# Kernel optimization log

Hardware: AMD Instinct MI355X
Metric: run time of the kernel (lower is better)

## Reference

```python
import jax, jax.numpy as jnp
import numpy as np

N, D, N_CLASSES = 8192, 512, 128
POS_MARGIN = 1.0  # default path: sample_method=None, Dynamic_margin=None


def setup_inputs() -> dict:
    key = jax.random.key(0)
    k1, k2 = jax.random.split(key)
    x = jax.random.normal(k1, (N, D), dtype=jnp.float32)
    # metric-learning embeddings are L2-normalized so sim in [-1, 1]
    x = x / jnp.linalg.norm(x, axis=1, keepdims=True)
    targets = jax.random.randint(k2, (N,), 0, N_CLASSES, dtype=jnp.int64)
    return {"inputs": x, "targets": targets, "nonorm": 0}


def reference(inputs, targets, nonorm):
    n = inputs.shape[0]
    sim = jnp.matmul(inputs, inputs.T)                      # [n, n]
    same = targets[:, None] == targets[None, :]             # [n, n]
    pos_mask = same & (sim < POS_MARGIN)                    # drops self-sim == 1
    neg_mask = ~same

    # per-row masked log-sum-exp (sort in original is irrelevant to the sums)
    pos_sum = jnp.sum(jnp.where(pos_mask, jnp.exp(1.0 - sim), 0.0), axis=1)
    neg_sum = jnp.sum(jnp.where(neg_mask, jnp.exp(sim), 0.0), axis=1)
    pos_loss = jnp.log(pos_sum)
    neg_loss = jnp.log(neg_sum)

    has_neg = jnp.any(neg_mask, axis=1)                     # rows w/o negs are skipped
    loss = jnp.sum(jnp.where(has_neg, pos_loss + neg_loss, 0.0)) / n
    prec = jnp.mean(1.0 - has_neg.astype(jnp.float32))      # fraction of skipped rows

    # torch code reports means of the LAST row's pos/neg pairs
    last_pos = pos_mask[-1]
    last_neg = neg_mask[-1]
    mean_pos_sim = jnp.sum(jnp.where(last_pos, sim[-1], 0.0)) / jnp.sum(last_pos)
    mean_neg_sim = jnp.sum(jnp.where(last_neg, sim[-1], 0.0)) / jnp.sum(last_neg)
    return loss, prec, mean_pos_sim, mean_neg_sim
```

## Files before the change

### kernel.cpp

```cpp
#include <hip/hip_runtime.h>
#include <math.h>

#define N_ 8192
#define D_ 512
#define NC_ 128
#define T32 32
#define BK_ 64
#define KSTEPS 8

typedef __attribute__((ext_vector_type(8))) short bf16x8;
typedef __attribute__((ext_vector_type(4))) float f32x4;
typedef __attribute__((ext_vector_type(4))) unsigned short us4;

static __device__ __forceinline__ unsigned short f2bf(float f) {
    union { float f; unsigned u; } c; c.f = f;
    unsigned u = c.u;
    u += 0x7fffu + ((u >> 16) & 1u);
    return (unsigned short)(u >> 16);
}

__global__ __launch_bounds__(256) void k_pre(const float* __restrict__ x,
                                             unsigned short* __restrict__ xb,
                                             const int* __restrict__ tg,
                                             double* __restrict__ sim_last,
                                             int* __restrict__ hist32,
                                             double* __restrict__ gd,
                                             int* __restrict__ gi) {
    const int bid = blockIdx.x;
    const int tid = threadIdx.x;
    if (bid == 0 && tid == 0) {
        atomicExch((unsigned long long*)&gd[0], 0ull);
        atomicExch((unsigned long long*)&gd[1], 0ull);
        atomicExch((unsigned long long*)&gd[2], 0ull);
        atomicExch(&gi[0], 0); atomicExch(&gi[1], 0);
        atomicExch(&gi[2], 0); atomicExch(&gi[3], 0);
    }
    if (bid < 4096) {
        int i = bid * 256 + tid;
        float4 v = reinterpret_cast<const float4*>(x)[i];
        us4 o = { f2bf(v.x), f2bf(v.y), f2bf(v.z), f2bf(v.w) };
        reinterpret_cast<us4*>(xb)[i] = o;
    } else if (bid < 6144) {
        int j    = (bid - 4096) * 4 + (tid >> 6);
        int lane = tid & 63;
        const float* xl = x + (size_t)(N_ - 1) * D_;
        const float* xj = x + (size_t)j * D_;
        double acc = 0.0;
#pragma unroll
        for (int it = 0; it < 8; ++it) {
            int k = it * 64 + lane;
            acc += (double)xl[k] * (double)xj[k];
        }
#pragma unroll
        for (int m = 32; m >= 1; m >>= 1) acc += __shfl_xor(acc, m, 64);
        if (lane == 0) sim_last[j] = acc;
    } else {
        __shared__ int lh[NC_];
        int b = bid - 6144;
        if (tid < NC_) lh[tid] = 0;
        __syncthreads();
        atomicAdd(&lh[tg[b * 256 + tid]], 1);
        __syncthreads();
        if (tid < NC_) hist32[b * NC_ + tid] = lh[tid];
    }
}

__global__ __launch_bounds__(512, 1) void k_main(const unsigned short* __restrict__ xb,
                                                 const int* __restrict__ tg,
                                                 float* __restrict__ bufP,
                                                 float* __restrict__ bufN) {
    __shared__ alignas(16) unsigned short As0_[2 * 256 * 64];
    __shared__ alignas(16) unsigned short Bs0_[2 * 256 * 64];

    const int tid  = threadIdx.x;
    const int w    = tid >> 6;
    const int lane = tid & 63;
    const int q    = lane >> 4;
    const int l15  = lane & 15;
    const int wrow = w >> 2;
    const int wcol = w & 3;

    const int bswz = (blockIdx.x & 7) * 66 + (blockIdx.x >> 3);

    int rem = bswz;
    int it = 0;
    while (rem >= (T32 - it)) { rem -= (T32 - it); it++; }
    const int jt = it + rem;
    const int row0 = it * 256;
    const int col0 = jt * 256;

    auto stage_tile = [&](int p, int kt) {
        const int k0 = kt * BK_;
#pragma unroll
        for (int set = 0; set < 4; ++set) {
            int ls = set * 4096 + tid * 8;
            int r  = ls >> 6;
            int sl = (ls >> 3) & 7;
            int g  = sl ^ (r & 7);
            const unsigned short* ga = xb + (size_t)(row0 + r) * D_ + k0 + g * 8;
            const unsigned short* gb = xb + (size_t)(col0 + r) * D_ + k0 + g * 8;
            __builtin_amdgcn_global_load_lds(
                (const __attribute__((address_space(1))) void*)ga,
                (__attribute__((address_space(3))) void*)(As0_ + p * 16384 + set * 4096 + w * 512),
                16, 0, 0);
            __builtin_amdgcn_global_load_lds(
                (const __attribute__((address_space(1))) void*)gb,
                (__attribute__((address_space(3))) void*)(Bs0_ + p * 16384 + set * 4096 + w * 512),
                16, 0, 0);
        }
    };

    f32x4 acc[8][4];
#pragma unroll
    for (int mi = 0; mi < 8; ++mi)
#pragma unroll
        for (int ni = 0; ni < 4; ++ni)
            acc[mi][ni] = (f32x4){0.f, 0.f, 0.f, 0.f};

    auto compute_kc = [&](int p, int kc) {
        bf16x8 aF[8], bF[4];
#pragma unroll
        for (int mi = 0; mi < 8; ++mi) {
            int rA = wrow * 128 + mi * 16 + l15;
            int sl = (kc * 4 + q) ^ (rA & 7);
            aF[mi] = *reinterpret_cast<const bf16x8*>(As0_ + p * 16384 + rA * 64 + sl * 8);
        }
#pragma unroll
        for (int ni = 0; ni < 4; ++ni) {
            int rB = wcol * 64 + ni * 16 + l15;
            int sl = (kc * 4 + q) ^ (rB & 7);
            bF[ni] = *reinterpret_cast<const bf16x8*>(Bs0_ + p * 16384 + rB * 64 + sl * 8);
        }
        asm volatile("s_waitcnt lgkmcnt(0)" ::: "memory");
        __builtin_amdgcn_sched_barrier(0);
        __builtin_amdgcn_s_setprio(1);
#pragma unroll
        for (int mi = 0; mi < 8; ++mi)
#pragma unroll
            for (int ni = 0; ni < 4; ++ni)
                acc[mi][ni] = __builtin_amdgcn_mfma_f32_16x16x32_bf16(
                    aF[mi], bF[ni], acc[mi][ni], 0, 0, 0);
        __builtin_amdgcn_s_setprio(0);
    };

#define TILE(P, KS, DOSTAGE, VMN)                                         \
    do {                                                                  \
        asm volatile("s_waitcnt vmcnt(" #VMN ")" ::: "memory");           \
        __builtin_amdgcn_s_barrier();                                     \
        __builtin_amdgcn_sched_barrier(0);                                \
        compute_kc(P, 0);                                                 \
        compute_kc(P, 1);                                                 \
        __builtin_amdgcn_s_barrier();                                     \
        __builtin_amdgcn_sched_barrier(0);                                \
        if (DOSTAGE) stage_tile(P, (KS) + 2);                             \
    } while (0)

    stage_tile(0, 0);
    stage_tile(1, 1);

    TILE(0, 0, 1, 8);
    TILE(1, 1, 1, 8);
    TILE(0, 2, 1, 8);
    TILE(1, 3, 1, 8);
    TILE(0, 4, 1, 8);
    TILE(1, 5, 1, 8);
    TILE(0, 6, 0, 8);
    TILE(1, 7, 0, 0);
#undef TILE

    int tC[4];
#pragma unroll
    for (int ni = 0; ni < 4; ++ni)
        tC[ni] = tg[col0 + wcol * 64 + ni * 16 + l15];

    float cps[4], cns[4];
#pragma unroll
    for (int ni = 0; ni < 4; ++ni) { cps[ni] = 0.f; cns[ni] = 0.f; }

    float* scr = (float*)As0_;

#pragma unroll
    for (int mi = 0; mi < 8; ++mi) {
        int tRv[4];
#pragma unroll
        for (int r = 0; r < 4; ++r)
            tRv[r] = tg[row0 + wrow * 128 + mi * 16 + q * 4 + r];
        float ps_[4] = {0.f, 0.f, 0.f, 0.f};
        float ns_[4] = {0.f, 0.f, 0.f, 0.f};
#pragma unroll
        for (int ni = 0; ni < 4; ++ni)
#pragma unroll
            for (int r = 0; r < 4; ++r) {
                float s = acc[mi][ni][r];
                bool same = (tRv[r] == tC[ni]);
                float e = __expf(same ? 1.0f - s : s);
                float pe = (same && (s < 1.0f)) ? e : 0.0f;
                float ne = same ? 0.0f : e;
                ps_[r] += pe; ns_[r] += ne;
                cps[ni] += pe; cns[ni] += ne;
            }
#pragma unroll
        for (int r = 0; r < 4; ++r) {
            float p = ps_[r];
            float n = ns_[r];
#pragma unroll
            for (int m = 1; m < 16; m <<= 1) {
                p += __shfl_xor(p, m, 64);
                n += __shfl_xor(n, m, 64);
            }
            if (l15 == 0) {
                int rloc = wrow * 128 + mi * 16 + q * 4 + r;
                scr[wcol * 256 + rloc]        = p;
                scr[1024 + wcol * 256 + rloc] = n;
            }
        }
    }

#pragma unroll
    for (int ni = 0; ni < 4; ++ni) {
        float p = cps[ni];
        float n = cns[ni];
        p += __shfl_xor(p, 16, 64); p += __shfl_xor(p, 32, 64);
        n += __shfl_xor(n, 16, 64); n += __shfl_xor(n, 32, 64);
        if (q == 0) {
            int cloc = wcol * 64 + ni * 16 + l15;
            scr[2048 + wrow * 256 + cloc] = p;
            scr[2560 + wrow * 256 + cloc] = n;
        }
    }
    __syncthreads();

    if (tid < 256) {
        int r = tid;
        size_t off = ((size_t)it * T32 + jt) * 256 + r;
        bufP[off] = scr[r] + scr[256 + r] + scr[512 + r] + scr[768 + r];
        bufN[off] = scr[1024 + r] + scr[1280 + r] + scr[1536 + r] + scr[1792 + r];
    } else if (jt != it) {
        int c = tid - 256;
        size_t off = ((size_t)jt * T32 + it) * 256 + c;
        bufP[off] = scr[2048 + c] + scr[2304 + c];
        bufN[off] = scr[2560 + c] + scr[2816 + c];
    }
}

__global__ __launch_bounds__(256) void k_post(const float* __restrict__ bufP,
                                              const float* __restrict__ bufN,
                                              const int* __restrict__ tg,
                                              const int* __restrict__ hist32,
                                              const double* __restrict__ sim_last,
                                              double* __restrict__ gd,
                                              int* __restrict__ gi,
                                              float* __restrict__ out) {
    __shared__ int lh[NC_];
    __shared__ float sv[256];
    __shared__ double Rd[256], Pd[256], Nd[256];
    __shared__ int Ri[256], Pc[256], Nc[256];
    const int t   = blockIdx.x;
    const int tid = threadIdx.x;

    if (tid < NC_) {
        int a = 0;
#pragma unroll
        for (int b = 0; b < 32; ++b) a += hist32[b * NC_ + tid];
        lh[tid] = a;
    }

    const int half = tid >> 7;
    const int r    = tid & 127;
    const int rt   = t >> 1;
    const int r256 = (t & 1) * 128 + r;
    const float* buf  = half ? bufN : bufP;
    const float* base = buf + (size_t)rt * T32 * 256 + r256;
    float s = 0.f;
#pragma unroll
    for (int o = 0; o < T32; ++o) s += base[o * 256];
    sv[tid] = s;
    __syncthreads();

    double rd = 0.0, pd = 0.0, nd = 0.0;
    int ri = 0, pc = 0, nc = 0;
    if (tid < 128) {
        int row = t * 128 + tid;
        bool ok = lh[tg[row]] < N_;
        rd = ok ? (double)(logf(sv[tid]) + logf(sv[128 + tid])) : 0.0;
        ri = ok ? 0 : 1;
        double sl = sim_last[row];
        int tlast = tg[N_ - 1];
        if (tg[row] == tlast) { if (sl < 1.0) { pd = sl; pc = 1; } }
        else                  { nd = sl; nc = 1; }
    }

    Rd[tid] = rd; Ri[tid] = ri;
    Pd[tid] = pd; Pc[tid] = pc;
    Nd[tid] = nd; Nc[tid] = nc;
    __syncthreads();
    for (int st = 128; st >= 1; st >>= 1) {
        if (tid < st) {
            Rd[tid] += Rd[tid + st]; Pd[tid] += Pd[tid + st]; Nd[tid] += Nd[tid + st];
            Ri[tid] += Ri[tid + st]; Pc[tid] += Pc[tid + st]; Nc[tid] += Nc[tid + st];
        }
        __syncthreads();
    }

    if (tid == 0) {
        atomicAdd(&gd[0], Rd[0]);
        atomicAdd(&gd[1], Pd[0]);
        atomicAdd(&gd[2], Nd[0]);
        atomicAdd(&gi[0], Ri[0]);
        atomicAdd(&gi[1], Pc[0]);
        atomicAdd(&gi[2], Nc[0]);
        __threadfence();
        int old = atomicAdd(&gi[3], 1);
        if (old == 63) {
            double A = atomicAdd(&gd[0], 0.0);
            double B = atomicAdd(&gd[1], 0.0);
            double C = atomicAdd(&gd[2], 0.0);
            int U = atomicAdd(&gi[0], 0);
            int V = atomicAdd(&gi[1], 0);
            int Y = atomicAdd(&gi[2], 0);
            out[0] = (float)(A / (double)N_);
            out[1] = (float)U / (float)N_;
            out[2] = (float)(B / (double)V);
            out[3] = (float)(C / (double)Y);
        }
    }
}

extern "C" void kernel_launch(void* const* d_in, const int* in_sizes, int n_in,
                              void* d_out, int out_size, void* d_ws, size_t ws_size,
                              hipStream_t stream) {
    const float* x  = (const float*)d_in[0];
    const int*   tg = (const int*)d_in[1];
    char* ws = (char*)d_ws;

    unsigned short* xb = (unsigned short*)ws;
    const size_t XB = (size_t)N_ * D_ * 2;
    float*  bufP = (float*)(ws + XB);
    float*  bufN = (float*)(ws + XB + (1u << 20));
    double* sim_last = (double*)(ws + XB + (2u << 20));
    int*    hist32   = (int*)(ws + XB + (2u << 20) + 65536);
    double* gd   = (double*)(ws + XB + (2u << 20) + 65536 + 16384);
    int*    gi   = (int*)(ws + XB + (2u << 20) + 65536 + 16384 + 64);

    const int nblk_tri = T32 * (T32 + 1) / 2;

    hipLaunchKernelGGL(k_pre, dim3(4096 + 2048 + 32), dim3(256), 0, stream,
                       x, xb, tg, sim_last, hist32, gd, gi);
    hipLaunchKernelGGL(k_main, dim3(nblk_tri), dim3(512), 0, stream, xb, tg, bufP, bufN);
    hipLaunchKernelGGL(k_post, dim3(64), dim3(256), 0, stream,
                       bufP, bufN, tg, hist32, sim_last, gd, gi, (float*)d_out);
}
```

Before: 162.0 us.

## Double k_main block to 16 waves, each computing a 64x64 sub-tile

The main Gram-matrix kernel now launches 1024 threads per block instead of 512. Each of 16 waves owns a 64x64 output sub-tile, so its accumulators shrink from 8x4 to 4x4 MFMA fragments and register pressure drops. Global-to-LDS staging is split across twice as many waves, and the vmcnt waits and column-reduction scratch layout are adjusted to match. The intent is more waves per CU to hide latency, at the cost of more LDS fragment reads per MFMA and a larger block to synchronise.

```diff
diff --git a/kernel.cpp b/kernel.cpp
--- a/kernel.cpp
+++ b/kernel.cpp
@@ -65,12 +65,12 @@
     }
 }
 
-__global__ __launch_bounds__(512, 1) void k_main(const unsigned short* __restrict__ xb,
-                                                 const int* __restrict__ tg,
-                                                 float* __restrict__ bufP,
-                                                 float* __restrict__ bufN) {
-    __shared__ alignas(16) unsigned short As0_[2 * 256 * 64];
-    __shared__ alignas(16) unsigned short Bs0_[2 * 256 * 64];
+__global__ __launch_bounds__(1024, 4) void k_main(const unsigned short* __restrict__ xb,
+                                                  const int* __restrict__ tg,
+                                                  float* __restrict__ bufP,
+                                                  float* __restrict__ bufN) {
+    __shared__ alignas(16) unsigned short As[2][256 * 64];
+    __shared__ alignas(16) unsigned short Bs[2][256 * 64];
 
     const int tid  = threadIdx.x;
     const int w    = tid >> 6;
@@ -92,55 +92,58 @@
     auto stage_tile = [&](int p, int kt) {
         const int k0 = kt * BK_;
 #pragma unroll
-        for (int set = 0; set < 4; ++set) {
-            int ls = set * 4096 + tid * 8;
-            int r  = ls >> 6;
-            int sl = (ls >> 3) & 7;
+        for (int set = 0; set < 2; ++set) {
+            int c  = (set * 16 + w) * 64 + lane;
+            int r  = c >> 3;
+            int sl = c & 7;
             int g  = sl ^ (r & 7);
             const unsigned short* ga = xb + (size_t)(row0 + r) * D_ + k0 + g * 8;
             const unsigned short* gb = xb + (size_t)(col0 + r) * D_ + k0 + g * 8;
             __builtin_amdgcn_global_load_lds(
                 (const __attribute__((address_space(1))) void*)ga,
-                (__attribute__((address_space(3))) void*)(As0_ + p * 16384 + set * 4096 + w * 512),
+                (__attribute__((address_space(3))) void*)(&As[p][0] + (set * 16 + w) * 512),
                 16, 0, 0);
             __builtin_amdgcn_global_load_lds(
                 (const __attribute__((address_space(1))) void*)gb,
-                (__attribute__((address_space(3))) void*)(Bs0_ + p * 16384 + set * 4096 + w * 512),
+                (__attribute__((address_space(3))) void*)(&Bs[p][0] + (set * 16 + w) * 512),
                 16, 0, 0);
         }
     };
 
-    f32x4 acc[8][4];
-#pragma unroll
-    for (int mi = 0; mi < 8; ++mi)
+    f32x4 acc[4][4];
+#pragma unroll
+    for (int mi = 0; mi < 4; ++mi)
 #pragma unroll
         for (int ni = 0; ni < 4; ++ni)
             acc[mi][ni] = (f32x4){0.f, 0.f, 0.f, 0.f};
 
-    auto compute_kc = [&](int p, int kc) {
-        bf16x8 aF[8], bF[4];
-#pragma unroll
-        for (int mi = 0; mi < 8; ++mi) {
-            int rA = wrow * 128 + mi * 16 + l15;
-            int sl = (kc * 4 + q) ^ (rA & 7);
-            aF[mi] = *reinterpret_cast<const bf16x8*>(As0_ + p * 16384 + rA * 64 + sl * 8);
-        }
-#pragma unroll
-        for (int ni = 0; ni < 4; ++ni) {
-            int rB = wcol * 64 + ni * 16 + l15;
-            int sl = (kc * 4 + q) ^ (rB & 7);
-            bF[ni] = *reinterpret_cast<const bf16x8*>(Bs0_ + p * 16384 + rB * 64 + sl * 8);
-        }
-        asm volatile("s_waitcnt lgkmcnt(0)" ::: "memory");
-        __builtin_amdgcn_sched_barrier(0);
-        __builtin_amdgcn_s_setprio(1);
-#pragma unroll
-        for (int mi = 0; mi < 8; ++mi)
-#pragma unroll
-            for (int ni = 0; ni < 4; ++ni)
-                acc[mi][ni] = __builtin_amdgcn_mfma_f32_16x16x32_bf16(
-                    aF[mi], bF[ni], acc[mi][ni], 0, 0, 0);
-        __builtin_amdgcn_s_setprio(0);
+    auto compute_tile = [&](int p) {
+#pragma unroll
+        for (int kc = 0; kc < 2; ++kc) {
+            bf16x8 aF[4], bF[4];
+#pragma unroll
+            for (int mi = 0; mi < 4; ++mi) {
+                int rA = wrow * 64 + mi * 16 + l15;
+                int sl = (kc * 4 + q) ^ (rA & 7);
+                aF[mi] = *reinterpret_cast<const bf16x8*>(&As[p][0] + rA * 64 + sl * 8);
+            }
+#pragma unroll
+            for (int ni = 0; ni < 4; ++ni) {
+                int rB = wcol * 64 + ni * 16 + l15;
+                int sl = (kc * 4 + q) ^ (rB & 7);
+                bF[ni] = *reinterpret_cast<const bf16x8*>(&Bs[p][0] + rB * 64 + sl * 8);
+            }
+            asm volatile("s_waitcnt lgkmcnt(0)" ::: "memory");
+            __builtin_amdgcn_sched_barrier(0);
+            __builtin_amdgcn_s_setprio(1);
+#pragma unroll
+            for (int mi = 0; mi < 4; ++mi)
+#pragma unroll
+                for (int ni = 0; ni < 4; ++ni)
+                    acc[mi][ni] = __builtin_amdgcn_mfma_f32_16x16x32_bf16(
+                        aF[mi], bF[ni], acc[mi][ni], 0, 0, 0);
+            __builtin_amdgcn_s_setprio(0);
+        }
     };
 
 #define TILE(P, KS, DOSTAGE, VMN)                                         \
@@ -148,8 +151,7 @@
         asm volatile("s_waitcnt vmcnt(" #VMN ")" ::: "memory");           \
         __builtin_amdgcn_s_barrier();                                     \
         __builtin_amdgcn_sched_barrier(0);                                \
-        compute_kc(P, 0);                                                 \
-        compute_kc(P, 1);                                                 \
+        compute_tile(P);                                                  \
         __builtin_amdgcn_s_barrier();                                     \
         __builtin_amdgcn_sched_barrier(0);                                \
         if (DOSTAGE) stage_tile(P, (KS) + 2);                             \
@@ -158,13 +160,13 @@
     stage_tile(0, 0);
     stage_tile(1, 1);
 
-    TILE(0, 0, 1, 8);
-    TILE(1, 1, 1, 8);
-    TILE(0, 2, 1, 8);
-    TILE(1, 3, 1, 8);
-    TILE(0, 4, 1, 8);
-    TILE(1, 5, 1, 8);
-    TILE(0, 6, 0, 8);
+    TILE(0, 0, 1, 4);
+    TILE(1, 1, 1, 4);
+    TILE(0, 2, 1, 4);
+    TILE(1, 3, 1, 4);
+    TILE(0, 4, 1, 4);
+    TILE(1, 5, 1, 4);
+    TILE(0, 6, 0, 4);
     TILE(1, 7, 0, 0);
 #undef TILE
 
@@ -177,14 +179,14 @@
 #pragma unroll
     for (int ni = 0; ni < 4; ++ni) { cps[ni] = 0.f; cns[ni] = 0.f; }
 
-    float* scr = (float*)As0_;
-
-#pragma unroll
-    for (int mi = 0; mi < 8; ++mi) {
+    float* scr = (float*)As;
+
+#pragma unroll
+    for (int mi = 0; mi < 4; ++mi) {
         int tRv[4];
 #pragma unroll
         for (int r = 0; r < 4; ++r)
-            tRv[r] = tg[row0 + wrow * 128 + mi * 16 + q * 4 + r];
+            tRv[r] = tg[row0 + wrow * 64 + mi * 16 + q * 4 + r];
         float ps_[4] = {0.f, 0.f, 0.f, 0.f};
         float ns_[4] = {0.f, 0.f, 0.f, 0.f};
 #pragma unroll
@@ -209,7 +211,7 @@
                 n += __shfl_xor(n, m, 64);
             }
             if (l15 == 0) {
-                int rloc = wrow * 128 + mi * 16 + q * 4 + r;
+                int rloc = wrow * 64 + mi * 16 + q * 4 + r;
                 scr[wcol * 256 + rloc]        = p;
                 scr[1024 + wcol * 256 + rloc] = n;
             }
@@ -225,7 +227,7 @@
         if (q == 0) {
             int cloc = wcol * 64 + ni * 16 + l15;
             scr[2048 + wrow * 256 + cloc] = p;
-            scr[2560 + wrow * 256 + cloc] = n;
+            scr[3072 + wrow * 256 + cloc] = n;
         }
     }
     __syncthreads();
@@ -235,11 +237,11 @@
         size_t off = ((size_t)it * T32 + jt) * 256 + r;
         bufP[off] = scr[r] + scr[256 + r] + scr[512 + r] + scr[768 + r];
         bufN[off] = scr[1024 + r] + scr[1280 + r] + scr[1536 + r] + scr[1792 + r];
-    } else if (jt != it) {
+    } else if (tid < 512 && jt != it) {
         int c = tid - 256;
         size_t off = ((size_t)jt * T32 + it) * 256 + c;
-        bufP[off] = scr[2048 + c] + scr[2304 + c];
-        bufN[off] = scr[2560 + c] + scr[2816 + c];
+        bufP[off] = scr[2048 + c] + scr[2304 + c] + scr[2560 + c] + scr[2816 + c];
+        bufN[off] = scr[3072 + c] + scr[3328 + c] + scr[3584 + c] + scr[3840 + c];
     }
 }
 
@@ -346,7 +348,7 @@
 
     hipLaunchKernelGGL(k_pre, dim3(4096 + 2048 + 32), dim3(256), 0, stream,
                        x, xb, tg, sim_last, hist32, gd, gi);
-    hipLaunchKernelGGL(k_main, dim3(nblk_tri), dim3(512), 0, stream, xb, tg, bufP, bufN);
+    hipLaunchKernelGGL(k_main, dim3(nblk_tri), dim3(1024), 0, stream, xb, tg, bufP, bufN);
     hipLaunchKernelGGL(k_post, dim3(64), dim3(256), 0, stream,
                        bufP, bufN, tg, hist32, sim_last, gd, gi, (float*)d_out);
 }
```

After: 153.6 us. -5.2%, faster.

## Split K-tile compute into four quadrant phases interleaved with partial prefetch

Applied to the files above, without the earlier changes.

Restructures the GEMM main loop so each K-tile is computed in four phases over sub-quadrants of the accumulator tile. The global-to-LDS loads for the tile after next are split into halves and issued between phases, as each region of the buffer stops being read. The goal is to overlap memory staging with MFMA work inside a tile instead of bunching all loads after a full tile compute. It adds more barriers per tile and depends on fine-grained ordering of LDS reads against overwrites, so a small mistake could cause hazards.

```diff
diff --git a/kernel.cpp b/kernel.cpp
--- a/kernel.cpp
+++ b/kernel.cpp
@@ -69,8 +69,8 @@
                                                  const int* __restrict__ tg,
                                                  float* __restrict__ bufP,
                                                  float* __restrict__ bufN) {
-    __shared__ alignas(16) unsigned short As0_[2 * 256 * 64];
-    __shared__ alignas(16) unsigned short Bs0_[2 * 256 * 64];
+    __shared__ alignas(16) unsigned short As[2][256 * 64];
+    __shared__ alignas(16) unsigned short Bs[2][256 * 64];
 
     const int tid  = threadIdx.x;
     const int w    = tid >> 6;
@@ -89,23 +89,33 @@
     const int row0 = it * 256;
     const int col0 = jt * 256;
 
-    auto stage_tile = [&](int p, int kt) {
+    auto stage_A = [&](int p, int kt, int half) {
         const int k0 = kt * BK_;
 #pragma unroll
-        for (int set = 0; set < 4; ++set) {
-            int ls = set * 4096 + tid * 8;
-            int r  = ls >> 6;
-            int sl = (ls >> 3) & 7;
-            int g  = sl ^ (r & 7);
-            const unsigned short* ga = xb + (size_t)(row0 + r) * D_ + k0 + g * 8;
-            const unsigned short* gb = xb + (size_t)(col0 + r) * D_ + k0 + g * 8;
+        for (int i = 0; i < 2; ++i) {
+            int c  = i * 512 + tid;
+            int rr = c >> 3, sl = c & 7;
+            int row = (rr & 63) + ((rr >> 6) << 7) + half * 64;
+            int g  = sl ^ (rr & 7);
+            const unsigned short* ga = xb + (size_t)(row0 + row) * D_ + k0 + g * 8;
             __builtin_amdgcn_global_load_lds(
                 (const __attribute__((address_space(1))) void*)ga,
-                (__attribute__((address_space(3))) void*)(As0_ + p * 16384 + set * 4096 + w * 512),
+                (__attribute__((address_space(3))) void*)(&As[p][0] + row * 64 + sl * 8),
                 16, 0, 0);
+        }
+    };
+    auto stage_B = [&](int p, int kt, int half) {
+        const int k0 = kt * BK_;
+#pragma unroll
+        for (int i = 0; i < 2; ++i) {
+            int c  = i * 512 + tid;
+            int rr = c >> 3, sl = c & 7;
+            int row = (rr & 31) + ((rr >> 5) << 6) + half * 32;
+            int g  = sl ^ (rr & 7);
+            const unsigned short* gb = xb + (size_t)(col0 + row) * D_ + k0 + g * 8;
             __builtin_amdgcn_global_load_lds(
                 (const __attribute__((address_space(1))) void*)gb,
-                (__attribute__((address_space(3))) void*)(Bs0_ + p * 16384 + set * 4096 + w * 512),
+                (__attribute__((address_space(3))) void*)(&Bs[p][0] + row * 64 + sl * 8),
                 16, 0, 0);
         }
     };
@@ -117,56 +127,94 @@
         for (int ni = 0; ni < 4; ++ni)
             acc[mi][ni] = (f32x4){0.f, 0.f, 0.f, 0.f};
 
-    auto compute_kc = [&](int p, int kc) {
-        bf16x8 aF[8], bF[4];
-#pragma unroll
-        for (int mi = 0; mi < 8; ++mi) {
-            int rA = wrow * 128 + mi * 16 + l15;
-            int sl = (kc * 4 + q) ^ (rA & 7);
-            aF[mi] = *reinterpret_cast<const bf16x8*>(As0_ + p * 16384 + rA * 64 + sl * 8);
-        }
-#pragma unroll
-        for (int ni = 0; ni < 4; ++ni) {
-            int rB = wcol * 64 + ni * 16 + l15;
-            int sl = (kc * 4 + q) ^ (rB & 7);
-            bF[ni] = *reinterpret_cast<const bf16x8*>(Bs0_ + p * 16384 + rB * 64 + sl * 8);
-        }
-        asm volatile("s_waitcnt lgkmcnt(0)" ::: "memory");
-        __builtin_amdgcn_sched_barrier(0);
-        __builtin_amdgcn_s_setprio(1);
-#pragma unroll
-        for (int mi = 0; mi < 8; ++mi)
-#pragma unroll
-            for (int ni = 0; ni < 4; ++ni)
-                acc[mi][ni] = __builtin_amdgcn_mfma_f32_16x16x32_bf16(
-                    aF[mi], bF[ni], acc[mi][ni], 0, 0, 0);
-        __builtin_amdgcn_s_setprio(0);
-    };
-
-#define TILE(P, KS, DOSTAGE, VMN)                                         \
-    do {                                                                  \
-        asm volatile("s_waitcnt vmcnt(" #VMN ")" ::: "memory");           \
-        __builtin_amdgcn_s_barrier();                                     \
-        __builtin_amdgcn_sched_barrier(0);                                \
-        compute_kc(P, 0);                                                 \
-        compute_kc(P, 1);                                                 \
-        __builtin_amdgcn_s_barrier();                                     \
-        __builtin_amdgcn_sched_barrier(0);                                \
-        if (DOSTAGE) stage_tile(P, (KS) + 2);                             \
+    bf16x8 a0[4][2], a1[4][2], b0[2][2], b1[2][2];
+
+#define RD_A(DST, P, MB)                                                      \
+    _Pragma("unroll")                                                         \
+    for (int mi2 = 0; mi2 < 4; ++mi2)                                         \
+        _Pragma("unroll")                                                     \
+        for (int kc = 0; kc < 2; ++kc) {                                      \
+            int rA = wrow * 128 + ((MB) + mi2) * 16 + l15;                    \
+            int sl = (kc * 4 + q) ^ (rA & 7);                                 \
+            DST[mi2][kc] = *reinterpret_cast<const bf16x8*>(                  \
+                &As[P][0] + rA * 64 + sl * 8);                                \
+        }
+#define RD_B(DST, P, NB)                                                      \
+    _Pragma("unroll")                                                         \
+    for (int ni2 = 0; ni2 < 2; ++ni2)                                         \
+        _Pragma("unroll")                                                     \
+        for (int kc = 0; kc < 2; ++kc) {                                      \
+            int rB = wcol * 64 + ((NB) + ni2) * 16 + l15;                     \
+            int sl = (kc * 4 + q) ^ (rB & 7);                                 \
+            DST[ni2][kc] = *reinterpret_cast<const bf16x8*>(                  \
+                &Bs[P][0] + rB * 64 + sl * 8);                                \
+        }
+#define QMFMA(AF, BF, MB, NB)                                                 \
+    _Pragma("unroll")                                                         \
+    for (int mi2 = 0; mi2 < 4; ++mi2)                                         \
+        _Pragma("unroll")                                                     \
+        for (int ni2 = 0; ni2 < 2; ++ni2)                                     \
+            _Pragma("unroll")                                                 \
+            for (int kc = 0; kc < 2; ++kc)                                    \
+                acc[(MB) + mi2][(NB) + ni2] =                                 \
+                    __builtin_amdgcn_mfma_f32_16x16x32_bf16(                  \
+                        AF[mi2][kc], BF[ni2][kc],                             \
+                        acc[(MB) + mi2][(NB) + ni2], 0, 0, 0);
+
+#define PH_BAR()                                                              \
+    __builtin_amdgcn_s_barrier();                                             \
+    __builtin_amdgcn_sched_barrier(0)
+#define PH_PRE()                                                              \
+    asm volatile("s_waitcnt lgkmcnt(0)" ::: "memory");                        \
+    __builtin_amdgcn_sched_barrier(0);                                        \
+    __builtin_amdgcn_s_setprio(1)
+#define PH_POST() __builtin_amdgcn_s_setprio(0)
+
+#define GROUP(P, KT2, DS)                                                     \
+    do {                                                                      \
+                                                                     \
+        PH_BAR();                                                             \
+        RD_A(a0, P, 0) RD_B(b0, P, 0)                                         \
+        PH_PRE(); QMFMA(a0, b0, 0, 0) PH_POST();                              \
+                                                                     \
+        PH_BAR();                                                             \
+        RD_B(b1, P, 2)                                                        \
+        if (DS) { stage_A(P, KT2, 0); stage_B(P, KT2, 0); }                   \
+        PH_PRE(); QMFMA(a0, b1, 0, 2) PH_POST();                              \
+                                                                     \
+        PH_BAR();                                                             \
+        RD_A(a1, P, 4)                                                        \
+        if (DS) stage_B(P, KT2, 1);                                           \
+        PH_PRE(); QMFMA(a1, b0, 4, 0) PH_POST();                              \
+                                                                     \
+        PH_BAR();                                                             \
+        if (DS) stage_A(P, KT2, 1);                                           \
+        __builtin_amdgcn_sched_barrier(0);                                    \
+        __builtin_amdgcn_s_setprio(1);                                        \
+        QMFMA(a1, b1, 4, 2)                                                   \
+        __builtin_amdgcn_s_setprio(0);                                        \
     } while (0)
 
-    stage_tile(0, 0);
-    stage_tile(1, 1);
-
-    TILE(0, 0, 1, 8);
-    TILE(1, 1, 1, 8);
-    TILE(0, 2, 1, 8);
-    TILE(1, 3, 1, 8);
-    TILE(0, 4, 1, 8);
-    TILE(1, 5, 1, 8);
-    TILE(0, 6, 0, 8);
-    TILE(1, 7, 0, 0);
-#undef TILE
+    stage_A(0, 0, 0); stage_B(0, 0, 0); stage_B(0, 0, 1); stage_A(0, 0, 1);
+    stage_A(1, 1, 0); stage_B(1, 1, 0); stage_B(1, 1, 1); stage_A(1, 1, 1);
+    asm volatile("s_waitcnt vmcnt(8)" ::: "memory");
+
+    GROUP(0, 2, 1); asm volatile("s_waitcnt vmcnt(8)" ::: "memory");
+    GROUP(1, 3, 1); asm volatile("s_waitcnt vmcnt(8)" ::: "memory");
+    GROUP(0, 4, 1); asm volatile("s_waitcnt vmcnt(8)" ::: "memory");
+    GROUP(1, 5, 1); asm volatile("s_waitcnt vmcnt(8)" ::: "memory");
+    GROUP(0, 6, 1); asm volatile("s_waitcnt vmcnt(8)" ::: "memory");
+    GROUP(1, 7, 1); asm volatile("s_waitcnt vmcnt(8)" ::: "memory");
+    GROUP(0, 9, 0); asm volatile("s_waitcnt vmcnt(0)" ::: "memory");
+    GROUP(1, 9, 0);
+
+#undef GROUP
+#undef PH_POST
+#undef PH_PRE
+#undef PH_BAR
+#undef QMFMA
+#undef RD_B
+#undef RD_A
 
     int tC[4];
 #pragma unroll
@@ -177,7 +225,7 @@
 #pragma unroll
     for (int ni = 0; ni < 4; ++ni) { cps[ni] = 0.f; cns[ni] = 0.f; }
 
-    float* scr = (float*)As0_;
+    float* scr = (float*)As;
 
 #pragma unroll
     for (int mi = 0; mi < 8; ++mi) {
```

Result: no change. 159.0 us (-1.9%).
